# Kernel optimization log

Hardware: AMD Instinct MI355X
Metric: run time of the kernel (lower is better)

The kernel has to match this reference:

```python
import jax, jax.numpy as jnp
import numpy as np

N, C, K, G, E = 65536, 256, 128, 32, 2097152
LN_EPS = 1e-5


def setup_inputs() -> dict:
    key = jax.random.key(0)
    ks = jax.random.split(key, 16)
    inp = {
        "x": jax.random.normal(ks[0], (N, C), jnp.float32),
        "evals_batch": jax.random.uniform(ks[1], (G * K,), jnp.float32),
        "evecs": jax.random.normal(ks[2], (N, K), jnp.float32),
        "mass": jax.random.uniform(ks[3], (N,), jnp.float32),
        "row": jax.random.randint(ks[4], (E,), 0, N),
        "col": jax.random.randint(ks[5], (E,), 0, N),
        "vals": jax.random.normal(ks[6], (E,), jnp.float32),
        # learned parameters (torch Linear convention: weight is [out, in])
        "t_params": jnp.full((C,), 0.5, jnp.float32),
        "grad_W": jax.random.normal(ks[7], (C, C), jnp.float32) / np.sqrt(C),
        "grad_b": jnp.zeros((C,), jnp.float32),
        "W1": jax.random.normal(ks[8], (C, 2 * C), jnp.float32) / np.sqrt(2 * C),
        "b1": jnp.zeros((C,), jnp.float32),
        "W2": jax.random.normal(ks[9], (C, C), jnp.float32) / np.sqrt(C),
        "b2": jnp.zeros((C,), jnp.float32),
        "ln_g": jnp.ones((C,), jnp.float32),
        "ln_b": jnp.zeros((C,), jnp.float32),
    }
    return inp


def reference(x, evals_batch, evecs, mass, row, col, vals,
              t_params, grad_W, grad_b, W1, b1, W2, b2, ln_g, ln_b):
    # batch is contiguous with G equal-size graphs of n nodes each
    n = N // G
    t = jnp.abs(t_params)                                   # [C]
    xg = x.reshape(G, n, C)
    eg = evecs.reshape(G, n, K)
    mg = mass.reshape(G, n)
    ev = evals_batch.reshape(G, K)
    # spectral diffusion, batched over graphs
    x_spec = jnp.einsum('gnk,gnc->gkc', eg, xg * mg[..., None])      # [G,K,C]
    decay = jnp.exp(-t[None, None, :] * jnp.clip(ev, 0.0)[..., None])  # [G,K,C]
    diff_out = jnp.einsum('gnk,gkc->gnc', eg, x_spec * decay).reshape(N, C)
    # sparse gradient operator: grad_feat = grad_X_sparse @ x  (COO)
    grad_feat = jax.ops.segment_sum(vals[:, None] * x[col], row, num_segments=N)
    grad_feat = grad_feat @ grad_W.T + grad_b
    # MLP (dropout is identity at eval)
    fused = jnp.concatenate([diff_out, grad_feat], axis=-1)           # [N,2C]
    h = jax.nn.relu(fused @ W1.T + b1)
    fused = h @ W2.T + b2
    # residual + LayerNorm
    y = x + fused
    mu = jnp.mean(y, axis=-1, keepdims=True)
    var = jnp.var(y, axis=-1, keepdims=True)
    return (y - mu) * jax.lax.rsqrt(var + LN_EPS) * ln_g + ln_b
```

## Files before the change

kernel.cpp:

```cpp
#include <hip/hip_runtime.h>

typedef unsigned short u16;
typedef unsigned long long u64;
using short8 = __attribute__((ext_vector_type(8))) short;
using f32x4  = __attribute__((ext_vector_type(4))) float;
using h16x4  = __attribute__((ext_vector_type(4))) _Float16;

constexpr int N_  = 65536;
constexpr int C_  = 256;
constexpr int K_  = 128;
constexpr int G_  = 32;
constexpr int NG_ = 2048;
constexpr int E_  = 2097152;
constexpr int NBIN_ = 2048;
constexpr int CAPB_ = 1280;
constexpr int NCHK_ = 256;

__device__ __forceinline__ u16 f2bf(float f) {
  unsigned u = __float_as_uint(f);
  unsigned r = u + 0x7FFF + ((u >> 16) & 1);
  return (u16)(r >> 16);
}
__device__ __forceinline__ float bf2f(u16 h) { return __uint_as_float((unsigned)h << 16); }
__device__ __forceinline__ u16 f2h(float f) {
  _Float16 h = (_Float16)f;
  u16 b; __builtin_memcpy(&b, &h, 2);
  return b;
}

__device__ __forceinline__ void gload_lds16(const void* g, void* l) {
  __builtin_amdgcn_global_load_lds((const __attribute__((address_space(1))) void*)g,
                                   (__attribute__((address_space(3))) void*)l, 16, 0, 0);
}

constexpr int EPI_BF16  = 0;
constexpr int EPI_DECAY = 3;
constexpr int EPI_TRANS = 4;

template <int BM, int BN, int EPI>
__device__ __forceinline__ void gemm_body(
    char* smem, int bx, int by, int z,
    const u16* __restrict__ A, long sAz, int lda,
    const u16* __restrict__ B, long sBz, int ldb,
    int Kd,
    void* __restrict__ outp, long sCz, int ldc,
    const float* __restrict__ tpar, const float* __restrict__ evptr) {
  constexpr int WM = BM / 2, WN = BN / 2;
  constexpr int FM = WM / 16, FN = WN / 16;
  u16* Asm = (u16*)smem;
  u16* Bsm = Asm + BM * 32;
  const u16* Ab = A + (long)z * sAz + (long)bx * BM * lda;
  const u16* Bb = B + (long)z * sBz + (long)by * BN * ldb;
  int tid = threadIdx.x;
  int wave = tid >> 6, lane = tid & 63;
  int wm = wave >> 1, wn = wave & 1;

  f32x4 acc[FM][FN];
  #pragma unroll
  for (int m = 0; m < FM; ++m)
    #pragma unroll
    for (int n = 0; n < FN; ++n) acc[m][n] = {0.f, 0.f, 0.f, 0.f};

  const u16* aA = Ab + (size_t)(wave * 16 + (lane >> 2)) * lda + (lane & 3) * 8;
  const u16* aB = Bb + (size_t)(wave * 16 + (lane >> 2)) * ldb + (lane & 3) * 8;
  u16* lA = Asm + wave * 512;
  u16* lB = Bsm + wave * 512;
  int arow = wm * WM + (lane & 15);
  int brow = wn * WN + (lane & 15);
  int kof = (lane >> 4) * 8;

  for (int k0 = 0; k0 < Kd; k0 += 32) {
    #pragma unroll
    for (int j = 0; j < BM / 64; ++j) gload_lds16(aA + (size_t)j * 64 * lda + k0, lA + j * 2048);
    #pragma unroll
    for (int j = 0; j < BN / 64; ++j) gload_lds16(aB + (size_t)j * 64 * ldb + k0, lB + j * 2048);
    __syncthreads();
    short8 af[FM], bfr[FN];
    #pragma unroll
    for (int m = 0; m < FM; ++m) af[m] = *(const short8*)(Asm + (arow + m * 16) * 32 + kof);
    #pragma unroll
    for (int n = 0; n < FN; ++n) bfr[n] = *(const short8*)(Bsm + (brow + n * 16) * 32 + kof);
    #pragma unroll
    for (int m = 0; m < FM; ++m)
      #pragma unroll
      for (int n = 0; n < FN; ++n)
        acc[m][n] = __builtin_amdgcn_mfma_f32_16x16x32_bf16(af[m], bfr[n], acc[m][n], 0, 0, 0);
    __syncthreads();
  }

  #pragma unroll
  for (int m = 0; m < FM; ++m) {
    #pragma unroll
    for (int n = 0; n < FN; ++n) {
      int cc = by * BN + wn * WN + n * 16 + (lane & 15);
      int rb = bx * BM + wm * WM + m * 16 + ((lane >> 4) << 2);
      if constexpr (EPI == EPI_TRANS) {
        ushort4 o = {f2bf(acc[m][n][0]), f2bf(acc[m][n][1]), f2bf(acc[m][n][2]), f2bf(acc[m][n][3])};
        *(ushort4*)((u16*)outp + (long)z * sCz + (long)cc * ldc + rb) = o;
      } else if constexpr (EPI == EPI_DECAY) {
        float tv = fabsf(tpar[cc]);
        #pragma unroll
        for (int r = 0; r < 4; ++r) {
          float ee = fmaxf(evptr[(size_t)z * K_ + rb + r], 0.f);
          ((u16*)outp)[(long)z * sCz + (long)(rb + r) * ldc + cc] = f2bf(acc[m][n][r] * __expf(-tv * ee));
        }
      } else {
        #pragma unroll
        for (int r = 0; r < 4; ++r)
          ((u16*)outp)[(long)z * sCz + (long)(rb + r) * ldc + cc] = f2bf(acc[m][n][r]);
      }
    }
  }
}

template <int BM, int BN, int EPI>
__global__ __launch_bounds__(256) void k_gemm(
    const u16* __restrict__ A, long sAz, int lda,
    const u16* __restrict__ B, long sBz, int ldb,
    int Kd,
    void* __restrict__ outp, long sCz, int ldc,
    const float* __restrict__ tpar, const float* __restrict__ evptr) {
  __shared__ __align__(16) char smem[(BM + BN) * 32 * 2];
  gemm_body<BM, BN, EPI>(smem, blockIdx.x, blockIdx.y, blockIdx.z,
                         A, sAz, lda, B, sBz, ldb, Kd, outp, sCz, ldc, tpar, evptr);
}

constexpr int PA_HIST = NCHK_;
constexpr int PA_CVX  = 4096;
constexpr int PA_CVE  = 2048;
constexpr int PA_W1   = 512;
constexpr int PA_W2   = 256;
constexpr int PA_T256 = 16;
constexpr int PA_BC   = 16;
constexpr int PA_TOTAL = PA_HIST + PA_CVX + PA_CVE + PA_W1 + PA_W2 + PA_T256 + PA_BC;

__global__ __launch_bounds__(256) void k_phaseA(
    const int* __restrict__ row, int* __restrict__ bh,
    const float* __restrict__ x, const float* __restrict__ mass,
    u16* __restrict__ xhf, u16* __restrict__ xmT,
    const float* __restrict__ evecs, u16* __restrict__ Ebf, u16* __restrict__ EbfT,
    const float* __restrict__ W1, u16* __restrict__ W1bf,
    const float* __restrict__ W2, u16* __restrict__ W2bf,
    const float* __restrict__ gW, u16* __restrict__ gWT,
    const float* __restrict__ gb, const float* __restrict__ b1, float* __restrict__ bc) {
  __shared__ __align__(16) char smem[64 * 65 * 4 + 256];
  float (*tile)[65] = (float(*)[65])smem;
  float* msm = (float*)(smem + 64 * 65 * 4);
  int id = blockIdx.x, tid = threadIdx.x;

  if (id < PA_HIST) {
    int* hist = (int*)smem;
    #pragma unroll
    for (int j = 0; j < 8; ++j) hist[tid + j * 256] = 0;
    __syncthreads();
    int e0 = id * 8192 + tid;
    #pragma unroll 4
    for (int i = 0; i < 32; ++i)
      atomicAdd(&hist[row[e0 + i * 256] >> 5], 1);
    __syncthreads();
    #pragma unroll
    for (int j = 0; j < 8; ++j) {
      int bin = tid + j * 256;
      bh[(size_t)bin * NCHK_ + id] = hist[bin];
    }
    return;
  }
  id -= PA_HIST;
  if (id < PA_CVX) {
    int r0 = (id >> 2) * 64, c0 = (id & 3) * 64;
    int tr = tid >> 4, tc4 = (tid & 15) * 4;
    #pragma unroll
    for (int p = 0; p < 4; ++p) {
      int r = p * 16 + tr;
      float4 v = *(const float4*)&x[(size_t)(r0 + r) * C_ + c0 + tc4];
      tile[r][tc4 + 0] = v.x; tile[r][tc4 + 1] = v.y; tile[r][tc4 + 2] = v.z; tile[r][tc4 + 3] = v.w;
      ushort4 o = {f2h(v.x), f2h(v.y), f2h(v.z), f2h(v.w)};
      *(ushort4*)&xhf[(size_t)(r0 + r) * C_ + c0 + tc4] = o;
    }
    if (tid < 64) msm[tid] = mass[r0 + tid];
    __syncthreads();
    int g = r0 >> 11, n0 = r0 & (NG_ - 1);
    #pragma unroll
    for (int p = 0; p < 4; ++p) {
      int cl = p * 16 + tr;
      ushort4 o;
      o.x = f2bf(tile[tc4 + 0][cl] * msm[tc4 + 0]);
      o.y = f2bf(tile[tc4 + 1][cl] * msm[tc4 + 1]);
      o.z = f2bf(tile[tc4 + 2][cl] * msm[tc4 + 2]);
      o.w = f2bf(tile[tc4 + 3][cl] * msm[tc4 + 3]);
      *(ushort4*)&xmT[((size_t)g * C_ + c0 + cl) * NG_ + n0 + tc4] = o;
    }
    return;
  }
  id -= PA_CVX;
  if (id < PA_CVE) {
    int r0 = (id >> 1) * 64, c0 = (id & 1) * 64;
    int tr = tid >> 4, tc4 = (tid & 15) * 4;
    #pragma unroll
    for (int p = 0; p < 4; ++p) {
      int r = p * 16 + tr;
      float4 v = *(const float4*)&evecs[(size_t)(r0 + r) * K_ + c0 + tc4];
      tile[r][tc4 + 0] = v.x; tile[r][tc4 + 1] = v.y; tile[r][tc4 + 2] = v.z; tile[r][tc4 + 3] = v.w;
      ushort4 o = {f2bf(v.x), f2bf(v.y), f2bf(v.z), f2bf(v.w)};
      *(ushort4*)&Ebf[(size_t)(r0 + r) * K_ + c0 + tc4] = o;
    }
    __syncthreads();
    int g = r0 >> 11, n0 = r0 & (NG_ - 1);
    #pragma unroll
    for (int p = 0; p < 4; ++p) {
      int cl = p * 16 + tr;
      ushort4 o = {f2bf(tile[tc4 + 0][cl]), f2bf(tile[tc4 + 1][cl]),
                   f2bf(tile[tc4 + 2][cl]), f2bf(tile[tc4 + 3][cl])};
      *(ushort4*)&EbfT[((size_t)g * K_ + c0 + cl) * NG_ + n0 + tc4] = o;
    }
    return;
  }
  id -= PA_CVE;
  if (id < PA_W1) { int i = id * 256 + tid; W1bf[i] = f2bf(W1[i]); return; }
  id -= PA_W1;
  if (id < PA_W2) { int i = id * 256 + tid; W2bf[i] = f2bf(W2[i]); return; }
  id -= PA_W2;
  if (id < PA_T256) {
    int r0 = (id & 3) * 64, c0 = (id >> 2) * 64;
    int tr = tid >> 4, tc4 = (tid & 15) * 4;
    #pragma unroll
    for (int p = 0; p < 4; ++p) {
      int r = p * 16 + tr;
      float4 v = *(const float4*)&gW[(size_t)(r0 + r) * 256 + c0 + tc4];
      tile[r][tc4 + 0] = v.x; tile[r][tc4 + 1] = v.y; tile[r][tc4 + 2] = v.z; tile[r][tc4 + 3] = v.w;
    }
    __syncthreads();
    #pragma unroll
    for (int p = 0; p < 4; ++p) {
      int cl = p * 16 + tr;
      ushort4 o = {f2bf(tile[tc4 + 0][cl]), f2bf(tile[tc4 + 1][cl]),
                   f2bf(tile[tc4 + 2][cl]), f2bf(tile[tc4 + 3][cl])};
      *(ushort4*)&gWT[(size_t)(c0 + cl) * 256 + r0 + tc4] = o;
    }
    return;
  }
  id -= PA_T256;
  {
    float* red = (float*)smem;
    int cl = tid >> 4, js = tid & 15;
    int c = id * 16 + cl;
    const float* wrow = &W1[(size_t)c * 512 + 256 + js * 16];
    float s = 0.f;
    #pragma unroll
    for (int jj = 0; jj < 16; ++jj) s += wrow[jj] * gb[js * 16 + jj];
    red[cl * 17 + js] = s;
    __syncthreads();
    if (js == 0) {
      float tot = b1[c];
      #pragma unroll
      for (int q = 0; q < 16; ++q) tot += red[cl * 17 + q];
      bc[c] = tot;
    }
  }
}

__global__ __launch_bounds__(256) void k_scanOS(const int* __restrict__ bh, int* __restrict__ baseL,
                                                int* __restrict__ gcnt) {
  __shared__ int sc[256];
  int bin = blockIdx.x, tid = threadIdx.x;
  int v = bh[(size_t)bin * NCHK_ + tid];
  sc[tid] = v;
  __syncthreads();
  for (int o = 1; o < 256; o <<= 1) {
    int t = (tid >= o) ? sc[tid - o] : 0;
    __syncthreads();
    sc[tid] += t;
    __syncthreads();
  }
  baseL[(size_t)tid * NBIN_ + bin] = sc[tid] - v;
  if (tid == 255) gcnt[bin] = sc[255];
}

constexpr int PB_SCAT = NCHK_;
constexpr int PB_WC   = 4;
constexpr int PB_SP1  = 128;
constexpr int PB_TOTAL = PB_SCAT + PB_WC + PB_SP1;

__global__ __launch_bounds__(256) void k_phaseB(
    const int* __restrict__ row, const int* __restrict__ col, const float* __restrict__ vals,
    const int* __restrict__ baseL, u64* __restrict__ epB,
    const u16* __restrict__ W1bf, const u16* __restrict__ gWT, u16* __restrict__ Wc,
    const u16* __restrict__ EbfT, const u16* __restrict__ xmT, u16* __restrict__ S,
    const float* __restrict__ tpar, const float* __restrict__ evptr) {
  __shared__ __align__(16) char smem[16384];
  int id = blockIdx.x, tid = threadIdx.x;

  if (id < PB_SCAT) {
    int* sbase = (int*)smem;
    int* cur   = sbase + NBIN_;
    #pragma unroll
    for (int j = 0; j < 8; ++j) {
      int b = tid + j * 256;
      sbase[b] = baseL[(size_t)id * NBIN_ + b];
      cur[b] = 0;
    }
    __syncthreads();
    int e0 = id * 8192 + tid;
    #pragma unroll 4
    for (int i = 0; i < 32; ++i) {
      int e = e0 + i * 256;
      int rr = row[e];
      int b = rr >> 5;
      int rk = atomicAdd(&cur[b], 1);
      int lpos = sbase[b] + rk;
      if (lpos < CAPB_)
        epB[(size_t)b * CAPB_ + lpos] =
            ((u64)(rr & 31) << 32) | ((u64)f2h(vals[e]) << 16) | (u64)(unsigned)col[e];
    }
    return;
  }
  id -= PB_SCAT;
  if (id < PB_WC) {
    gemm_body<128, 128, EPI_BF16>(smem, id & 1, id >> 1, 0,
                                  W1bf + 256, 0, 512, gWT, 0, 256, 256,
                                  Wc, 0, 256, nullptr, nullptr);
    return;
  }
  id -= PB_WC;
  {
    int zz = id >> 2, rem = id & 3;
    gemm_body<64, 128, EPI_DECAY>(smem, rem & 1, rem >> 1, zz,
                                  EbfT, (long)K_ * NG_, NG_, xmT, (long)C_ * NG_, NG_, NG_,
                                  S, (long)K_ * C_, C_, tpar, evptr);
  }
}

__global__ __launch_bounds__(256) void k_gatherF(const u16* __restrict__ xhf, const int* __restrict__ gcnt,
                                                 const u64* __restrict__ epB, u16* __restrict__ gf) {
  __shared__ unsigned eL[CAPB_];
  __shared__ int chist[256];
  __shared__ int roff[257];
  __shared__ int sc[256];
  int b = blockIdx.x, tid = threadIdx.x;
  int wave = tid >> 6, lane = tid & 63;
  int n = gcnt[b]; if (n > CAPB_) n = CAPB_;
  chist[tid] = 0;
  __syncthreads();
  const u64* ebase = epB + (size_t)b * CAPB_;
  unsigned pkr[5]; int cellr[5]; int rkr[5];
  #pragma unroll
  for (int q = 0; q < 5; ++q) {
    int i = tid + q * 256;
    bool ok = i < n;
    u64 pk = ok ? ebase[i] : 0;
    int cell = (int)((pk & 0xFFFFu) >> 13) * 32 + ((int)(pk >> 32) & 31);
    pkr[q] = (unsigned)pk; cellr[q] = cell; rkr[q] = 0;
    if (ok) rkr[q] = atomicAdd(&chist[cell], 1);
  }
  __syncthreads();
  int s = chist[tid];
  sc[tid] = s;
  __syncthreads();
  for (int o = 1; o < 256; o <<= 1) {
    int v = (tid >= o) ? sc[tid - o] : 0;
    __syncthreads();
    sc[tid] += v;
    __syncthreads();
  }
  roff[tid] = sc[tid] - s;
  if (tid == 255) roff[256] = sc[255];
  __syncthreads();
  #pragma unroll
  for (int q = 0; q < 5; ++q) {
    int i = tid + q * 256;
    if (i < n) eL[roff[cellr[q]] + rkr[q]] = pkr[q];
  }
  __syncthreads();

  const u16* xb = xhf + lane * 4;
  f32x4 acc[8];
  #pragma unroll
  for (int k = 0; k < 8; ++k) acc[k] = {0.f, 0.f, 0.f, 0.f};
  for (int t = 0; t < 8; ++t) {
    #pragma unroll
    for (int k = 0; k < 8; ++k) {
      int cell = t * 32 + wave * 8 + k;
      int j = roff[cell], en = roff[cell + 1];
      while (j < en) {
        unsigned u[4]; h16x4 xv[4];
        #pragma unroll
        for (int q = 0; q < 4; ++q) u[q] = (j + q < en) ? eL[j + q] : 0u;
        #pragma unroll
        for (int q = 0; q < 4; ++q) xv[q] = *(const h16x4*)(xb + (size_t)(u[q] & 0xFFFFu) * C_);
        #pragma unroll
        for (int q = 0; q < 4; ++q) {
          u16 hb = (u16)(u[q] >> 16);
          _Float16 hv; __builtin_memcpy(&hv, &hb, 2);
          float v = (float)hv;
          acc[k][0] += (float)xv[q][0] * v;
          acc[k][1] += (float)xv[q][1] * v;
          acc[k][2] += (float)xv[q][2] * v;
          acc[k][3] += (float)xv[q][3] * v;
        }
        j += 4;
      }
    }
    __syncthreads();
  }
  int r0 = b * 32 + wave * 8;
  #pragma unroll
  for (int k = 0; k < 8; ++k) {
    ushort4 o = {f2bf(acc[k][0]), f2bf(acc[k][1]), f2bf(acc[k][2]), f2bf(acc[k][3])};
    *(ushort4*)&gf[(size_t)(r0 + k) * C_ + lane * 4] = o;
  }
}

__global__ __launch_bounds__(256) void k_mlp(
    const u16* __restrict__ Eb, const u16* __restrict__ Tt,
    const u16* __restrict__ gf, const u16* __restrict__ Wc,
    const float* __restrict__ bc,
    const u16* __restrict__ W2bf, const float* __restrict__ b2,
    const float* __restrict__ x, const float* __restrict__ lng, const float* __restrict__ lnb,
    float* __restrict__ out) {
  __shared__ __align__(16) u16 Asm[64 * 32];
  __shared__ __align__(16) u16 Bsm[256 * 32];
  __shared__ __align__(16) u16 hs[64 * 256];
  __shared__ float ps1[64][4], ps2[64][4];
  int i0 = blockIdx.x * 64;
  int g = i0 >> 11;
  int tid = threadIdx.x, wave = tid >> 6, lane = tid & 63;
  int wn = wave;
  int srow = wave * 16 + (lane >> 2), scol = (lane & 3) * 8;
  u16* lA = Asm + wave * 512;
  u16* lB = Bsm + wave * 512;
  int arow = lane & 15;
  int brow = wn * 64 + (lane & 15);
  int kof = (lane >> 4) * 8;

  f32x4 acc[4][4];
  #pragma unroll
  for (int m = 0; m < 4; ++m)
    #pragma unroll
    for (int n = 0; n < 4; ++n) acc[m][n] = {0.f, 0.f, 0.f, 0.f};

  {
    const u16* aA = Eb + (size_t)(i0 + srow) * K_ + scol;
    const u16* aB = Tt + (size_t)g * C_ * K_ + (size_t)srow * K_ + scol;
    for (int k0 = 0; k0 < 128; k0 += 32) {
      gload_lds16(aA + k0, lA);
      #pragma unroll
      for (int j = 0; j < 4; ++j) gload_lds16(aB + (size_t)j * 64 * K_ + k0, lB + j * 2048);
      __syncthreads();
      short8 af[4], bfr[4];
      #pragma unroll
      for (int m = 0; m < 4; ++m) af[m] = *(const short8*)(Asm + (arow + m * 16) * 32 + kof);
      #pragma unroll
      for (int n = 0; n < 4; ++n) bfr[n] = *(const short8*)(Bsm + (brow + n * 16) * 32 + kof);
      #pragma unroll
      for (int m = 0; m < 4; ++m)
        #pragma unroll
        for (int n = 0; n < 4; ++n)
          acc[m][n] = __builtin_amdgcn_mfma_f32_16x16x32_bf16(af[m], bfr[n], acc[m][n], 0, 0, 0);
      __syncthreads();
    }
  }
  {
    const u16* aA = gf + (size_t)(i0 + srow) * C_ + scol;
    const u16* aB = Wc + (size_t)srow * C_ + scol;
    for (int k0 = 0; k0 < 256; k0 += 32) {
      gload_lds16(aA + k0, lA);
      #pragma unroll
      for (int j = 0; j < 4; ++j) gload_lds16(aB + (size_t)j * 64 * C_ + k0, lB + j * 2048);
      __syncthreads();
      short8 af[4], bfr[4];
      #pragma unroll
      for (int m = 0; m < 4; ++m) af[m] = *(const short8*)(Asm + (arow + m * 16) * 32 + kof);
      #pragma unroll
      for (int n = 0; n < 4; ++n) bfr[n] = *(const short8*)(Bsm + (brow + n * 16) * 32 + kof);
      #pragma unroll
      for (int m = 0; m < 4; ++m)
        #pragma unroll
        for (int n = 0; n < 4; ++n)
          acc[m][n] = __builtin_amdgcn_mfma_f32_16x16x32_bf16(af[m], bfr[n], acc[m][n], 0, 0, 0);
      __syncthreads();
    }
  }
  #pragma unroll
  for (int n = 0; n < 4; ++n) {
    int cc = wn * 64 + n * 16 + (lane & 15);
    float bv = bc[cc];
    #pragma unroll
    for (int m = 0; m < 4; ++m) {
      #pragma unroll
      for (int r = 0; r < 4; ++r) {
        int rb = m * 16 + ((lane >> 4) << 2) + r;
        hs[(rb * 256 + cc) ^ ((rb & 7) << 3)] = f2bf(fmaxf(acc[m][n][r] + bv, 0.f));
      }
    }
  }
  __syncthreads();

  #pragma unroll
  for (int m = 0; m < 4; ++m)
    #pragma unroll
    for (int n = 0; n < 4; ++n) acc[m][n] = {0.f, 0.f, 0.f, 0.f};
  {
    const u16* aB = W2bf + (size_t)srow * C_ + scol;
    for (int k0 = 0; k0 < 256; k0 += 32) {
      #pragma unroll
      for (int j = 0; j < 4; ++j) gload_lds16(aB + (size_t)j * 64 * C_ + k0, lB + j * 2048);
      __syncthreads();
      short8 af[4], bfr[4];
      #pragma unroll
      for (int m = 0; m < 4; ++m) {
        int ar = arow + m * 16;
        af[m] = *(const short8*)(hs + ((ar * 256 + k0 + kof) ^ ((ar & 7) << 3)));
      }
      #pragma unroll
      for (int n = 0; n < 4; ++n) bfr[n] = *(const short8*)(Bsm + (brow + n * 16) * 32 + kof);
      #pragma unroll
      for (int m = 0; m < 4; ++m)
        #pragma unroll
        for (int n = 0; n < 4; ++n)
          acc[m][n] = __builtin_amdgcn_mfma_f32_16x16x32_bf16(af[m], bfr[n], acc[m][n], 0, 0, 0);
      __syncthreads();
    }
  }
  float bb[4], lg[4], lb[4];
  #pragma unroll
  for (int n = 0; n < 4; ++n) {
    int cc = wn * 64 + n * 16 + (lane & 15);
    bb[n] = b2[cc]; lg[n] = lng[cc]; lb[n] = lnb[cc];
  }
  #pragma unroll
  for (int m = 0; m < 4; ++m) {
    #pragma unroll
    for (int r = 0; r < 4; ++r) {
      int rl = m * 16 + ((lane >> 4) << 2) + r;
      #pragma unroll
      for (int n = 0; n < 4; ++n) {
        int cc = wn * 64 + n * 16 + (lane & 15);
        acc[m][n][r] += bb[n] + x[(size_t)(i0 + rl) * C_ + cc];
      }
    }
  }
  #pragma unroll
  for (int m = 0; m < 4; ++m) {
    #pragma unroll
    for (int r = 0; r < 4; ++r) {
      float t1 = acc[m][0][r] + acc[m][1][r] + acc[m][2][r] + acc[m][3][r];
      float t2 = acc[m][0][r] * acc[m][0][r] + acc[m][1][r] * acc[m][1][r] +
                 acc[m][2][r] * acc[m][2][r] + acc[m][3][r] * acc[m][3][r];
      #pragma unroll
      for (int msk = 1; msk < 16; msk <<= 1) {
        t1 += __shfl_xor(t1, msk);
        t2 += __shfl_xor(t2, msk);
      }
      if ((lane & 15) == 0) {
        int rl = m * 16 + ((lane >> 4) << 2) + r;
        ps1[rl][wn] = t1; ps2[rl][wn] = t2;
      }
    }
  }
  __syncthreads();
  #pragma unroll
  for (int m = 0; m < 4; ++m) {
    #pragma unroll
    for (int r = 0; r < 4; ++r) {
      int rl = m * 16 + ((lane >> 4) << 2) + r;
      float tot1 = ps1[rl][0] + ps1[rl][1] + ps1[rl][2] + ps1[rl][3];
      float tot2 = ps2[rl][0] + ps2[rl][1] + ps2[rl][2] + ps2[rl][3];
      float mu = tot1 * (1.f / 256.f);
      float var = fmaxf(tot2 * (1.f / 256.f) - mu * mu, 0.f);
      float rs = rsqrtf(var + 1e-5f);
      #pragma unroll
      for (int n = 0; n < 4; ++n) {
        int cc = wn * 64 + n * 16 + (lane & 15);
        out[(size_t)(i0 + rl) * C_ + cc] = (acc[m][n][r] - mu) * rs * lg[n] + lb[n];
      }
    }
  }
}

extern "C" void kernel_launch(void* const* d_in, const int* in_sizes, int n_in,
                              void* d_out, int out_size, void* d_ws, size_t ws_size,
                              hipStream_t stream) {
  const float* x        = (const float*)d_in[0];
  const float* ev       = (const float*)d_in[1];
  const float* evecs    = (const float*)d_in[2];
  const float* mass     = (const float*)d_in[3];
  const int*   row      = (const int*)d_in[4];
  const int*   col      = (const int*)d_in[5];
  const float* vals     = (const float*)d_in[6];
  const float* t_params = (const float*)d_in[7];
  const float* gW       = (const float*)d_in[8];
  const float* gb       = (const float*)d_in[9];
  const float* W1       = (const float*)d_in[10];
  const float* b1       = (const float*)d_in[11];
  const float* W2       = (const float*)d_in[12];
  const float* b2       = (const float*)d_in[13];
  const float* lng      = (const float*)d_in[14];
  const float* lnb      = (const float*)d_in[15];
  float* out = (float*)d_out;

  char* p = (char*)d_ws;
  u16* xhf  = (u16*)p; p += (size_t)N_ * C_ * 2;
  u16* xmT  = (u16*)p; p += (size_t)G_ * C_ * NG_ * 2;
  u16* EbfT = (u16*)p; p += (size_t)G_ * K_ * NG_ * 2;
  u16* Ebf  = (u16*)p; p += (size_t)N_ * K_ * 2;
  u16* S    = (u16*)p; p += (size_t)G_ * K_ * C_ * 2;
  u16* Tt   = (u16*)p; p += (size_t)G_ * C_ * K_ * 2;
  u16* W1bf = (u16*)p; p += (size_t)C_ * 512 * 2;
  u16* W2bf = (u16*)p; p += (size_t)C_ * C_ * 2;
  u16* gWT  = (u16*)p; p += (size_t)C_ * C_ * 2;
  u16* Wc   = (u16*)p; p += (size_t)C_ * C_ * 2;
  float* bc = (float*)p; p += (size_t)C_ * 4;
  int* gcnt = (int*)p; p += (size_t)NBIN_ * 4;
  int* bh   = (int*)p; p += (size_t)NBIN_ * NCHK_ * 4;
  int* baseL= (int*)p; p += (size_t)NCHK_ * NBIN_ * 4;
  u64* epB  = (u64*)p; p += (size_t)NBIN_ * CAPB_ * 8;
  u16* gf   = xmT;

  k_phaseA<<<PA_TOTAL, 256, 0, stream>>>(row, bh, x, mass, xhf, xmT,
                                         evecs, Ebf, EbfT, W1, W1bf, W2, W2bf,
                                         gW, gWT, gb, b1, bc);
  k_scanOS<<<NBIN_, 256, 0, stream>>>(bh, baseL, gcnt);
  k_phaseB<<<PB_TOTAL, 256, 0, stream>>>(row, col, vals, baseL, epB,
                                         W1bf, gWT, Wc, EbfT, xmT, S, t_params, ev);
  k_gemm<128, 128, EPI_TRANS><<<dim3(1, 2, G_), 256, 0, stream>>>(
      S, (long)K_ * C_, C_, W1bf, 0, 512, 256,
      Tt, (long)C_ * K_, K_, nullptr, nullptr);

  k_gatherF<<<NBIN_, 256, 0, stream>>>(xhf, gcnt, epB, gf);

  k_mlp<<<N_ / 64, 256, 0, stream>>>(Ebf, Tt, gf, Wc, bc, W2bf, b2, x, lng, lnb, out);
}
```

Before: 323.4 us.

## Move spectral projection GEMM into gather kernel to overlap with sparse gather

Moves the per-graph spectral projection GEMM (with decay epilogue) out of the scatter kernel and into the same launch as the sparse gather, so the 128 GEMM blocks run alongside the 2048 gather blocks. The gather output gets its own workspace buffer instead of aliasing xmT, because xmT is now read by the GEMM while the gather writes. The aim is to balance load across phases and fill idle CUs. The cost is extra workspace memory, and shared memory is now carved manually.

```diff
diff --git a/kernel.cpp b/kernel.cpp
--- a/kernel.cpp
+++ b/kernel.cpp
@@ -278,15 +278,12 @@
 
 constexpr int PB_SCAT = NCHK_;
 constexpr int PB_WC   = 4;
-constexpr int PB_SP1  = 128;
-constexpr int PB_TOTAL = PB_SCAT + PB_WC + PB_SP1;
+constexpr int PB_TOTAL = PB_SCAT + PB_WC;
 
 __global__ __launch_bounds__(256) void k_phaseB(
     const int* __restrict__ row, const int* __restrict__ col, const float* __restrict__ vals,
     const int* __restrict__ baseL, u64* __restrict__ epB,
-    const u16* __restrict__ W1bf, const u16* __restrict__ gWT, u16* __restrict__ Wc,
-    const u16* __restrict__ EbfT, const u16* __restrict__ xmT, u16* __restrict__ S,
-    const float* __restrict__ tpar, const float* __restrict__ evptr) {
+    const u16* __restrict__ W1bf, const u16* __restrict__ gWT, u16* __restrict__ Wc) {
   __shared__ __align__(16) char smem[16384];
   int id = blockIdx.x, tid = threadIdx.x;
 
@@ -315,28 +312,34 @@
     return;
   }
   id -= PB_SCAT;
-  if (id < PB_WC) {
-    gemm_body<128, 128, EPI_BF16>(smem, id & 1, id >> 1, 0,
-                                  W1bf + 256, 0, 512, gWT, 0, 256, 256,
-                                  Wc, 0, 256, nullptr, nullptr);
-    return;
-  }
-  id -= PB_WC;
-  {
-    int zz = id >> 2, rem = id & 3;
+  gemm_body<128, 128, EPI_BF16>(smem, id & 1, id >> 1, 0,
+                                W1bf + 256, 0, 512, gWT, 0, 256, 256,
+                                Wc, 0, 256, nullptr, nullptr);
+}
+
+constexpr int PC_TOTAL = NBIN_ + 128;
+
+__global__ __launch_bounds__(256) void k_phaseC(
+    const u16* __restrict__ xhf, const int* __restrict__ gcnt,
+    const u64* __restrict__ epB, u16* __restrict__ gf,
+    const u16* __restrict__ EbfT, const u16* __restrict__ xmT, u16* __restrict__ S,
+    const float* __restrict__ tpar, const float* __restrict__ evptr) {
+  __shared__ __align__(16) char smem[12544];
+  int id = blockIdx.x, tid = threadIdx.x;
+
+  if (id >= NBIN_) {
+    int sid = id - NBIN_;
+    int zz = sid >> 2, rem = sid & 3;
     gemm_body<64, 128, EPI_DECAY>(smem, rem & 1, rem >> 1, zz,
                                   EbfT, (long)K_ * NG_, NG_, xmT, (long)C_ * NG_, NG_, NG_,
                                   S, (long)K_ * C_, C_, tpar, evptr);
-  }
-}
-
-__global__ __launch_bounds__(256) void k_gatherF(const u16* __restrict__ xhf, const int* __restrict__ gcnt,
-                                                 const u64* __restrict__ epB, u16* __restrict__ gf) {
-  __shared__ unsigned eL[CAPB_];
-  __shared__ int chist[256];
-  __shared__ int roff[257];
-  __shared__ int sc[256];
-  int b = blockIdx.x, tid = threadIdx.x;
+    return;
+  }
+  int b = id;
+  unsigned* eL = (unsigned*)smem;
+  int* chist = (int*)(smem + 5120);
+  int* roff  = chist + 256;
+  int* sc    = roff + 257;
   int wave = tid >> 6, lane = tid & 63;
   int n = gcnt[b]; if (n > CAPB_) n = CAPB_;
   chist[tid] = 0;
@@ -605,6 +608,7 @@
   u16* Ebf  = (u16*)p; p += (size_t)N_ * K_ * 2;
   u16* S    = (u16*)p; p += (size_t)G_ * K_ * C_ * 2;
   u16* Tt   = (u16*)p; p += (size_t)G_ * C_ * K_ * 2;
+  u16* gf   = (u16*)p; p += (size_t)N_ * C_ * 2;
   u16* W1bf = (u16*)p; p += (size_t)C_ * 512 * 2;
   u16* W2bf = (u16*)p; p += (size_t)C_ * C_ * 2;
   u16* gWT  = (u16*)p; p += (size_t)C_ * C_ * 2;
@@ -614,19 +618,16 @@
   int* bh   = (int*)p; p += (size_t)NBIN_ * NCHK_ * 4;
   int* baseL= (int*)p; p += (size_t)NCHK_ * NBIN_ * 4;
   u64* epB  = (u64*)p; p += (size_t)NBIN_ * CAPB_ * 8;
-  u16* gf   = xmT;
 
   k_phaseA<<<PA_TOTAL, 256, 0, stream>>>(row, bh, x, mass, xhf, xmT,
                                          evecs, Ebf, EbfT, W1, W1bf, W2, W2bf,
                                          gW, gWT, gb, b1, bc);
   k_scanOS<<<NBIN_, 256, 0, stream>>>(bh, baseL, gcnt);
-  k_phaseB<<<PB_TOTAL, 256, 0, stream>>>(row, col, vals, baseL, epB,
-                                         W1bf, gWT, Wc, EbfT, xmT, S, t_params, ev);
+  k_phaseB<<<PB_TOTAL, 256, 0, stream>>>(row, col, vals, baseL, epB, W1bf, gWT, Wc);
+  k_phaseC<<<PC_TOTAL, 256, 0, stream>>>(xhf, gcnt, epB, gf, EbfT, xmT, S, t_params, ev);
   k_gemm<128, 128, EPI_TRANS><<<dim3(1, 2, G_), 256, 0, stream>>>(
       S, (long)K_ * C_, C_, W1bf, 0, 512, 256,
       Tt, (long)C_ * K_, K_, nullptr, nullptr);
 
-  k_gatherF<<<NBIN_, 256, 0, stream>>>(xhf, gcnt, epB, gf);
-
   k_mlp<<<N_ / 64, 256, 0, stream>>>(Ebf, Tt, gf, Wc, bc, W2bf, b2, x, lng, lnb, out);
 }
```

Result: no change. 321.8 us (-0.5%).
